# Kernel tuning notes

Hardware: AMD Instinct MI355X
Metric: run time of the kernel (lower is better)

The kernel has to match this reference:

```python
import jax, jax.numpy as jnp
import numpy as np

BATCH, SEQ, H, P, HID, CHUNK = 2, 2048, 32, 64, 2048, 256
NORM_EPS = 1e-5


def setup_inputs() -> dict:
    key = jax.random.key(0)
    ks = jax.random.split(key, 10)
    f = lambda k, sh, sc=1.0: jax.random.normal(k, sh, jnp.float32) * sc
    return {
        "hidden_states_ab": f(ks[0], (BATCH, SEQ, HID), 0.02),
        "hidden_states_g": f(ks[1], (BATCH, SEQ, HID), 0.02),
        "q_states": f(ks[2], (BATCH, SEQ, H, P)),
        "k_states": f(ks[3], (BATCH, SEQ, H, P)),
        "v_states": f(ks[4], (BATCH, SEQ, H, P)),
        "dt_w": f(ks[5], (HID, H), 0.02),
        "dt_b": jnp.zeros((H,), jnp.float32),
        "g_w": f(ks[6], (HID, H), 0.02),
        "g_b": jnp.zeros((H,), jnp.float32),
        "A_log": jnp.log(jnp.arange(1, H + 1, dtype=jnp.float32)),
        "dt_bias": jnp.ones((H,), jnp.float32),
        "norm_weight": jnp.ones((H * P,), jnp.float32),
        "o_w": f(ks[7], (H, P, P), 0.02),
        "o_b": jnp.zeros((H, P), jnp.float32),
    }


def _l2norm(x, eps=1e-12):
    # torch F.normalize(p=2, dim=-1): x / max(||x||, eps)
    n = jnp.sqrt(jnp.sum(x * x, axis=-1, keepdims=True))
    return x / jnp.maximum(n, eps)


def _ssd(x, dt, A, Bm, Cm, chunk):
    # x: (b,s,h,p)  dt: (b,s,h) post-softplus  A: (h,)  Bm/Cm: (b,s,h,n)
    b, s, h, p = x.shape
    n = Bm.shape[-1]
    c = s // chunk
    rs = lambda t: t.reshape(b, c, chunk, *t.shape[2:])
    x, dt, Bm, Cm = rs(x), rs(dt), rs(Bm), rs(Cm)
    a = dt * A                         # (b,c,L,h) log-decay increments
    cum = jnp.cumsum(a, axis=2)        # (b,c,L,h)
    cumT = jnp.swapaxes(cum, 2, 3)     # (b,c,h,L)
    # intra-chunk (quadratic, causal) part
    diff = cumT[..., :, None] - cumT[..., None, :]          # (b,c,h,L,L)
    mask = jnp.tril(jnp.ones((chunk, chunk), bool))
    decay = jnp.exp(jnp.where(mask, diff, -jnp.inf))
    CB = jnp.einsum('bclhn,bcshn->bchls', Cm, Bm)
    scores = CB * decay * jnp.swapaxes(dt, 2, 3)[:, :, :, None, :]
    y = jnp.einsum('bchls,bcshp->bclhp', scores, x)
    # per-chunk states
    decay_last = jnp.exp(cumT[..., -1:] - cumT)             # (b,c,h,L)
    w = jnp.swapaxes(decay_last, 2, 3) * dt                 # (b,c,L,h)
    states = jnp.einsum('bclh,bclhn,bclhp->bchpn', w, Bm, x)
    # inter-chunk recurrence over c chunks
    chunk_decay = jnp.exp(cumT[..., -1])                    # (b,c,h)
    def step(Hs, inp):
        cd, st = inp
        return cd[..., None, None] * Hs + st, Hs
    H_last, H_prev = jax.lax.scan(
        step, jnp.zeros((b, h, p, n), x.dtype),
        (jnp.moveaxis(chunk_decay, 1, 0), jnp.moveaxis(states, 1, 0)))
    H_prev = jnp.moveaxis(H_prev, 0, 1)                     # (b,c,h,p,n)
    y = y + jnp.einsum('bclhn,bclh,bchpn->bclhp', Cm, jnp.exp(cum), H_prev)
    return y.reshape(b, s, h, p), H_last


def reference(hidden_states_ab, hidden_states_g, q_states, k_states, v_states,
              dt_w, dt_b, g_w, g_b, A_log, dt_bias, norm_weight, o_w, o_b):
    b, s, h, p = v_states.shape
    Cm = _l2norm(q_states)
    Bm = _l2norm(k_states)
    # dt_proj bias + mamba dt_bias, then softplus (dt_softplus=True)
    dt = jax.nn.softplus(hidden_states_ab @ dt_w + dt_b + dt_bias)   # (b,s,h)
    A = -jnp.exp(A_log)
    y, ssm_state = _ssd(v_states, dt, A, Bm, Cm, CHUNK)
    # gate: g_proj then repeat_interleave(head_dim) on last dim
    gate = jnp.repeat(hidden_states_g @ g_w + g_b, p, axis=-1)       # (b,s,h*p)
    # RMSNormGated, norm_before_gate=False: normalize(x * silu(z)) * weight
    y = y.reshape(b, s, h * p) * jax.nn.silu(gate)
    y = y * jax.lax.rsqrt(jnp.mean(y * y, axis=-1, keepdims=True) + NORM_EPS)
    y = y * norm_weight
    # GroupLinear o_proj: per-head (p -> p) linear
    out = jnp.einsum('bshp,hpq->bshq', y.reshape(b, s, h, p), o_w) + o_b
    return out.reshape(b, s, h * p)
```

## Files before the change

kernel.cpp:

```cpp
#include <hip/hip_runtime.h>
#include <math.h>

#define BATCH 2
#define SEQ   2048
#define NH    32
#define HID   2048
#define CHUNK 256
#define NCH   8
#define NBCH  (BATCH*NCH*NH)
#define PST   72
#define BK    256
#define APST  264
#define KSPLIT 4
#define KSEG  (HID / KSPLIT)

typedef __attribute__((ext_vector_type(4))) float f32x4;
typedef __attribute__((ext_vector_type(8))) short bf16x8;
typedef unsigned int uint;
typedef unsigned short ushort;

__device__ __forceinline__ float softplusf(float x) {
    return x > 20.f ? x : log1pf(expf(x));
}

__device__ __forceinline__ short f2bf(float f) {
    union { float f; uint u; } v; v.f = f;
    uint r = v.u + 0x7FFF + ((v.u >> 16) & 1);
    return (short)(r >> 16);
}
__device__ __forceinline__ float bf2f(ushort s) {
    union { uint u; float f; } v; v.u = ((uint)s) << 16; return v.f;
}
__device__ __forceinline__ uint packbf2(float lo, float hi) {
    return (uint)(ushort)f2bf(lo) | ((uint)(ushort)f2bf(hi) << 16);
}

struct BF8 { union { bf16x8 v; short s[8]; }; };

__device__ __forceinline__ bf16x8 load_cvt8(const float* p, float scale) {
    float4 a = *(const float4*)p;
    float4 b = *(const float4*)(p + 4);
    BF8 r;
    r.s[0]=f2bf(a.x*scale); r.s[1]=f2bf(a.y*scale); r.s[2]=f2bf(a.z*scale); r.s[3]=f2bf(a.w*scale);
    r.s[4]=f2bf(b.x*scale); r.s[5]=f2bf(b.y*scale); r.s[6]=f2bf(b.z*scale); r.s[7]=f2bf(b.w*scale);
    return r.v;
}

__device__ __forceinline__ bf16x8 cvt8(float4 a, float4 b, float s) {
    BF8 r;
    r.s[0]=f2bf(a.x*s); r.s[1]=f2bf(a.y*s); r.s[2]=f2bf(a.z*s); r.s[3]=f2bf(a.w*s);
    r.s[4]=f2bf(b.x*s); r.s[5]=f2bf(b.y*s); r.s[6]=f2bf(b.z*s); r.s[7]=f2bf(b.w*s);
    return r.v;
}

#define MFMA(a,b,c) __builtin_amdgcn_mfma_f32_16x16x32_bf16((a),(b),(c),0,0,0)

__global__ __launch_bounds__(256) void k_proj(
    const float* __restrict__ hs_ab, const float* __restrict__ hs_g,
    const float* __restrict__ dt_w, const float* __restrict__ g_w,
    const float* __restrict__ o_w,  const float* __restrict__ norm_w,
    float* __restrict__ part, short* __restrict__ nwWT)
{
    __shared__ __align__(16) short As[32 * APST];
    __shared__ __align__(16) short Bs[32 * APST];
    int blk = blockIdx.x;
    int t = threadIdx.x;

    if (blk >= 2 * KSPLIT * 128) {
        int h = blk - 2 * KSPLIT * 128;
        float* tile = (float*)As;
        {
            int p = t >> 2, q0 = (t & 3) * 16;
            const float* wp = o_w + (size_t)h * 4096 + p * 64 + q0;
            #pragma unroll
            for (int i = 0; i < 4; ++i)
                *(float4*)(tile + p * 64 + q0 + i * 4) = *(const float4*)(wp + i * 4);
        }
        __syncthreads();
        int q = t >> 2, p0 = (t & 3) * 16;
        uint us[8];
        #pragma unroll
        for (int j = 0; j < 8; ++j) {
            float lo = tile[(p0 + 2*j    ) * 64 + q] * norm_w[h * 64 + p0 + 2*j];
            float hi = tile[(p0 + 2*j + 1) * 64 + q] * norm_w[h * 64 + p0 + 2*j + 1];
            us[j] = packbf2(lo, hi);
        }
        uint* dst = (uint*)(nwWT + (size_t)h * 4096 + q * 64 + p0);
        *(uint4*)dst       = make_uint4(us[0], us[1], us[2], us[3]);
        *(uint4*)(dst + 4) = make_uint4(us[4], us[5], us[6], us[7]);
        return;
    }

    int ksp = blk >> 8;
    int rem = blk & 255;
    int which = rem >> 7;
    int rt = rem & 127;
    int r0 = rt * 32;
    const float* Am = which ? hs_g : hs_ab;
    const float* W  = which ? g_w  : dt_w;
    int w = t >> 6, lane = t & 63, quad = lane >> 4, l16 = lane & 15;
    int mh = w & 1, nh = w >> 1;

    f32x4 acc = (f32x4){0.f, 0.f, 0.f, 0.f};

    for (int kc = ksp * KSEG; kc < ksp * KSEG + KSEG; kc += BK) {
        __syncthreads();
        {
            int row = t >> 3, k0 = (t & 7) * 32;
            const float* src = Am + (size_t)(r0 + row) * HID + kc + k0;
            uint* dst = (uint*)(As + row * APST + k0);
            #pragma unroll
            for (int i = 0; i < 4; ++i) {
                float4 a = *(const float4*)(src + i * 8);
                float4 b = *(const float4*)(src + i * 8 + 4);
                dst[i*4+0] = packbf2(a.x, a.y); dst[i*4+1] = packbf2(a.z, a.w);
                dst[i*4+2] = packbf2(b.x, b.y); dst[i*4+3] = packbf2(b.z, b.w);
            }
        }
        if (t < 128) {
            int k2 = t * 2;
            const float* w0 = W + (size_t)(kc + k2) * NH;
            const float* w1 = w0 + NH;
            #pragma unroll
            for (int n = 0; n < 32; n += 4) {
                float4 a = *(const float4*)(w0 + n);
                float4 b = *(const float4*)(w1 + n);
                *((uint*)(Bs + (n+0) * APST + k2)) = packbf2(a.x, b.x);
                *((uint*)(Bs + (n+1) * APST + k2)) = packbf2(a.y, b.y);
                *((uint*)(Bs + (n+2) * APST + k2)) = packbf2(a.z, b.z);
                *((uint*)(Bs + (n+3) * APST + k2)) = packbf2(a.w, b.w);
            }
        }
        __syncthreads();
        #pragma unroll
        for (int ks = 0; ks < BK / 32; ++ks) {
            bf16x8 af = *(const bf16x8*)(As + (mh*16 + l16) * APST + ks*32 + quad*8);
            bf16x8 bf = *(const bf16x8*)(Bs + (nh*16 + l16) * APST + ks*32 + quad*8);
            acc = MFMA(af, bf, acc);
        }
    }

    int n = nh * 16 + l16;
    int Rb = r0 + mh * 16 + quad * 4;
    float* pd = part + ((size_t)(which * KSPLIT + ksp) * 4096 + Rb) * 32 + n;
    #pragma unroll
    for (int r = 0; r < 4; ++r)
        pd[r * 32] = acc[r];
}

__global__ __launch_bounds__(256) void k_cumsum(
    const float* __restrict__ part, const float* __restrict__ dt_b,
    const float* __restrict__ dt_bias, const float* __restrict__ A_log,
    float* __restrict__ cumc, float* __restrict__ wvc,
    float* __restrict__ dtc, float* __restrict__ cd)
{
    __shared__ float wsum[4];
    int bch = blockIdx.x;
    int h = bch & 31, c = (bch >> 5) & 7, b = bch >> 8;
    int t = threadIdx.x;
    int w = t >> 6, lane = t & 63;
    int rid = (b * SEQ + c * CHUNK + t) * 32 + h;
    float s = part[rid] + part[131072 + rid] + part[262144 + rid] + part[393216 + rid];
    float dt_l = softplusf(s + dt_b[h] + dt_bias[h]);
    float A = -expf(A_log[h]);
    float v = dt_l * A;
    #pragma unroll
    for (int off = 1; off < 64; off <<= 1) {
        float u = __shfl_up(v, off);
        if (lane >= off) v += u;
    }
    if (lane == 63) wsum[w] = v;
    __syncthreads();
    float pre = 0.f;
    #pragma unroll
    for (int i = 0; i < 3; ++i)
        if (i < w) pre += wsum[i];
    float cum = v + pre;
    float tot = wsum[0] + wsum[1] + wsum[2] + wsum[3];
    size_t o = (size_t)bch * CHUNK + t;
    cumc[o] = cum;
    wvc[o] = expf(tot - cum) * dt_l;
    dtc[o] = dt_l;
    if (t == 255) cd[bch] = expf(tot);
}

__global__ __launch_bounds__(256) void k_states(
    const float* __restrict__ kst, const float* __restrict__ vst,
    const float* __restrict__ wvc, float* __restrict__ sp)
{
    __shared__ __align__(16) float kS[64 * 64];
    __shared__ __align__(16) float xS[64 * 64];
    int blk = blockIdx.x;
    int half = blk & 1, bch = blk >> 1;
    int h = bch & 31, c = (bch >> 5) & 7, b = bch >> 8;
    int t = threadIdx.x;
    size_t rowbase = (size_t)b * SEQ + c * CHUNK + half * 128;
    int pg = (t & 15) * 4, ng = (t >> 4) * 4;
    float acc[4][4];
    #pragma unroll
    for (int i = 0; i < 4; ++i)
        #pragma unroll
        for (int j = 0; j < 4; ++j) acc[i][j] = 0.f;

    for (int tt = 0; tt < 2; ++tt) {
        int r0 = t >> 4;
        int c4 = (t & 15) * 4;
        #pragma unroll
        for (int i = 0; i < 4; ++i) {
            int row = r0 + i * 16;
            size_t grow = (rowbase + tt * 64 + row) * NH + h;
            float wv = wvc[(size_t)bch * CHUNK + half * 128 + tt * 64 + row];
            float4 kv = *(const float4*)(kst + grow * 64 + c4);
            float4 xv = *(const float4*)(vst + grow * 64 + c4);
            float ssq = kv.x*kv.x + kv.y*kv.y + kv.z*kv.z + kv.w*kv.w;
            ssq += __shfl_xor(ssq, 1); ssq += __shfl_xor(ssq, 2);
            ssq += __shfl_xor(ssq, 4); ssq += __shfl_xor(ssq, 8);
            float ib = 1.f / fmaxf(sqrtf(ssq), 1e-12f);
            *(float4*)(kS + row * 64 + c4) =
                make_float4(kv.x * ib, kv.y * ib, kv.z * ib, kv.w * ib);
            *(float4*)(xS + row * 64 + c4) =
                make_float4(xv.x * wv, xv.y * wv, xv.z * wv, xv.w * wv);
        }
        __syncthreads();
        for (int ll = 0; ll < 64; ++ll) {
            float4 x4 = *(const float4*)(xS + ll * 64 + pg);
            float4 k4 = *(const float4*)(kS + ll * 64 + ng);
            acc[0][0] += x4.x * k4.x; acc[0][1] += x4.x * k4.y;
            acc[0][2] += x4.x * k4.z; acc[0][3] += x4.x * k4.w;
            acc[1][0] += x4.y * k4.x; acc[1][1] += x4.y * k4.y;
            acc[1][2] += x4.y * k4.z; acc[1][3] += x4.y * k4.w;
            acc[2][0] += x4.z * k4.x; acc[2][1] += x4.z * k4.y;
            acc[2][2] += x4.z * k4.z; acc[2][3] += x4.z * k4.w;
            acc[3][0] += x4.w * k4.x; acc[3][1] += x4.w * k4.y;
            acc[3][2] += x4.w * k4.z; acc[3][3] += x4.w * k4.w;
        }
        __syncthreads();
    }
    size_t obase = (size_t)blk * 4096;
    #pragma unroll
    for (int i = 0; i < 4; ++i)
        *(float4*)(sp + obase + (pg + i) * 64 + ng) =
            make_float4(acc[i][0], acc[i][1], acc[i][2], acc[i][3]);
}

__global__ __launch_bounds__(256) void k_scan(
    const float* __restrict__ sp, const float* __restrict__ cd,
    float* __restrict__ Hp)
{
    size_t id = (size_t)blockIdx.x * 256 + threadIdx.x;
    size_t bh = id >> 12, pn = id & 4095;
    size_t b = bh >> 5, h = bh & 31;
    float carry = 0.f;
    for (int c = 0; c < NCH; ++c) {
        size_t bch = (b * NCH + c) * NH + h;
        float st = sp[(bch * 2) * 4096 + pn] + sp[(bch * 2 + 1) * 4096 + pn];
        Hp[bch * 4096 + pn] = carry;
        carry = cd[bch] * carry + st;
    }
}

__global__ __launch_bounds__(256, 2) void k_intra(
    const float* __restrict__ qst, const float* __restrict__ kst,
    const float* __restrict__ vst,
    const float* __restrict__ cumc, const float* __restrict__ dtc,
    const float* __restrict__ Hp,
    short* __restrict__ ygb)
{
    __shared__ __align__(16) short B_s[64 * PST];
    __shared__ __align__(16) short XT_s[64 * PST];
    __shared__ __align__(16) short P_s[4 * 32 * PST];
    __shared__ float sCum[256];
    __shared__ float sDt[256];

    int blk = blockIdx.x;
    int grp = (blk < NBCH) ? 0 : 1;
    int bch = blk & (NBCH - 1);
    int h = bch & 31, c = (bch >> 5) & 7, b = bch >> 8;
    int t = threadIdx.x;
    int w = t >> 6, lane = t & 63;
    int quad = lane >> 4, l16 = lane & 15;
    int strip = grp ? (1 + (w & 1) + 4 * (w >> 1))
                    : (3 * (w & 1) + 4 * (w >> 1));
    size_t rowbase = (size_t)b * SEQ + c * CHUNK;

    sCum[t] = cumc[(size_t)bch * CHUNK + t];
    sDt[t]  = dtc[(size_t)bch * CHUNK + t];

    int ssA = t >> 2, q4A = (t & 3) * 16;
    int ss2 = t & 31, p0 = (t >> 5) * 8;

    bf16x8 cf[2][2];
    #pragma unroll
    for (int lt = 0; lt < 2; ++lt) {
        int l = strip * 32 + lt * 16 + l16;
        size_t grow = (rowbase + l) * NH + h;
        const float* qp = qst + grow * 64 + quad * 8;
        float4 a  = *(const float4*)qp;
        float4 bq = *(const float4*)(qp + 4);
        float4 c2 = *(const float4*)(qp + 32);
        float4 d  = *(const float4*)(qp + 36);
        float ssq = a.x*a.x + a.y*a.y + a.z*a.z + a.w*a.w
                  + bq.x*bq.x + bq.y*bq.y + bq.z*bq.z + bq.w*bq.w
                  + c2.x*c2.x + c2.y*c2.y + c2.z*c2.z + c2.w*c2.w
                  + d.x*d.x + d.y*d.y + d.z*d.z + d.w*d.w;
        ssq += __shfl_xor(ssq, 16);
        ssq += __shfl_xor(ssq, 32);
        float ic = 1.f / fmaxf(sqrtf(ssq), 1e-12f);
        cf[lt][0] = cvt8(a, bq, ic);
        cf[lt][1] = cvt8(c2, d, ic);
    }

    f32x4 acc[2][4];
    #pragma unroll
    for (int lt = 0; lt < 2; ++lt)
        #pragma unroll
        for (int pt = 0; pt < 4; ++pt)
            acc[lt][pt] = (f32x4){0.f, 0.f, 0.f, 0.f};

    {
        bf16x8 hf[4][2];
        #pragma unroll
        for (int pt = 0; pt < 4; ++pt) {
            const float* hp = Hp + (size_t)bch * 4096 + (pt * 16 + l16) * 64 + quad * 8;
            hf[pt][0] = load_cvt8(hp, 1.f);
            hf[pt][1] = load_cvt8(hp + 32, 1.f);
        }
        #pragma unroll
        for (int lt = 0; lt < 2; ++lt)
            #pragma unroll
            for (int pt = 0; pt < 4; ++pt) {
                acc[lt][pt] = MFMA(cf[lt][0], hf[pt][0], acc[lt][pt]);
                acc[lt][pt] = MFMA(cf[lt][1], hf[pt][1], acc[lt][pt]);
            }
    }
    __syncthreads();
    #pragma unroll
    for (int lt = 0; lt < 2; ++lt) {
        float e[4];
        #pragma unroll
        for (int r = 0; r < 4; ++r)
            e[r] = __expf(sCum[strip * 32 + lt * 16 + quad * 4 + r]);
        #pragma unroll
        for (int pt = 0; pt < 4; ++pt)
            #pragma unroll
            for (int r = 0; r < 4; ++r)
                acc[lt][pt][r] *= e[r];
    }

    short* Pw = P_s + w * 32 * PST;

    for (int st = 0; st < 4; ++st) {
        {
            size_t gK = (rowbase + st * 64 + ssA) * NH + h;
            const float4* kp = (const float4*)(kst + gK * 64 + q4A);
            float4 kv0 = kp[0], kv1 = kp[1], kv2 = kp[2], kv3 = kp[3];
            float ssq = kv0.x*kv0.x + kv0.y*kv0.y + kv0.z*kv0.z + kv0.w*kv0.w
                      + kv1.x*kv1.x + kv1.y*kv1.y + kv1.z*kv1.z + kv1.w*kv1.w
                      + kv2.x*kv2.x + kv2.y*kv2.y + kv2.z*kv2.z + kv2.w*kv2.w
                      + kv3.x*kv3.x + kv3.y*kv3.y + kv3.z*kv3.z + kv3.w*kv3.w;
            ssq += __shfl_xor(ssq, 1);
            ssq += __shfl_xor(ssq, 2);
            float ib = 1.f / fmaxf(sqrtf(ssq), 1e-12f);
            uint u[8];
            u[0] = packbf2(kv0.x * ib, kv0.y * ib); u[1] = packbf2(kv0.z * ib, kv0.w * ib);
            u[2] = packbf2(kv1.x * ib, kv1.y * ib); u[3] = packbf2(kv1.z * ib, kv1.w * ib);
            u[4] = packbf2(kv2.x * ib, kv2.y * ib); u[5] = packbf2(kv2.z * ib, kv2.w * ib);
            u[6] = packbf2(kv3.x * ib, kv3.y * ib); u[7] = packbf2(kv3.z * ib, kv3.w * ib);
            uint* dst = (uint*)(B_s + ssA * PST + q4A);
            *(uint4*)dst = make_uint4(u[0], u[1], u[2], u[3]);
            *(uint4*)(dst + 4) = make_uint4(u[4], u[5], u[6], u[7]);
        }
        {
            size_t g0 = (rowbase + st * 64 + 2 * ss2) * NH + h;
            const float* vp0 = vst + g0 * 64 + p0;
            const float* vp1 = vst + (g0 + NH) * 64 + p0;
            float4 xa0 = *(const float4*)vp0, xa1 = *(const float4*)(vp0 + 4);
            float4 xb0 = *(const float4*)vp1, xb1 = *(const float4*)(vp1 + 4);
            float dt0 = sDt[st * 64 + 2 * ss2];
            float dt1 = sDt[st * 64 + 2 * ss2 + 1];
            float x0[8] = {xa0.x, xa0.y, xa0.z, xa0.w, xa1.x, xa1.y, xa1.z, xa1.w};
            float x1[8] = {xb0.x, xb0.y, xb0.z, xb0.w, xb1.x, xb1.y, xb1.z, xb1.w};
            uint* xt = (uint*)XT_s;
            #pragma unroll
            for (int i = 0; i < 8; ++i)
                xt[(p0 + i) * (PST / 2) + ss2] = packbf2(x0[i] * dt0, x1[i] * dt1);
        }
        __syncthreads();

        if (strip * 32 + 31 >= st * 64) {
            bf16x8 xf[4][2];
            #pragma unroll
            for (int pt = 0; pt < 4; ++pt) {
                #pragma unroll
                for (int ks = 0; ks < 2; ++ks)
                    xf[pt][ks] = *(const bf16x8*)(XT_s + (pt * 16 + l16) * PST + ks * 32 + quad * 8);
            }

            #pragma unroll
            for (int lt = 0; lt < 2; ++lt) {
                int Lt = strip * 32 + lt * 16;
                float cl = sCum[Lt + l16];
                int lrow = lt * 16 + l16;
                #pragma unroll
                for (int mt = 0; mt < 4; ++mt) {
                    int S0 = st * 64 + mt * 16;
                    uint* pdst = (uint*)(Pw + lrow * PST + mt * 16 + quad * 4);
                    if (S0 > Lt + 15) {
                        *(uint2*)pdst = make_uint2(0u, 0u);
                        continue;
                    }
                    f32x4 sa = (f32x4){0.f, 0.f, 0.f, 0.f};
                    bf16x8 af0 = *(const bf16x8*)(B_s + (mt * 16 + l16) * PST + quad * 8);
                    bf16x8 af1 = *(const bf16x8*)(B_s + (mt * 16 + l16) * PST + 32 + quad * 8);
                    sa = MFMA(af0, cf[lt][0], sa);
                    sa = MFMA(af1, cf[lt][1], sa);
                    float vals[4];
                    #pragma unroll
                    for (int r = 0; r < 4; ++r) {
                        int s = S0 + quad * 4 + r;
                        float v = sa[r] * __expf(cl - sCum[s]);
                        vals[r] = (Lt + l16 >= s) ? v : 0.f;
                    }
                    *(uint2*)pdst = make_uint2(packbf2(vals[0], vals[1]),
                                               packbf2(vals[2], vals[3]));
                }
            }
            #pragma unroll
            for (int lt = 0; lt < 2; ++lt) {
                int Lmax = strip * 32 + lt * 16 + 15;
                #pragma unroll
                for (int ks = 0; ks < 2; ++ks) {
                    if (st * 64 + ks * 32 > Lmax) continue;
                    bf16x8 af = *(const bf16x8*)(Pw + (lt * 16 + l16) * PST + ks * 32 + quad * 8);
                    #pragma unroll
                    for (int pt = 0; pt < 4; ++pt)
                        acc[lt][pt] = MFMA(af, xf[pt][ks], acc[lt][pt]);
                }
            }
        }
        __syncthreads();
    }

    #pragma unroll
    for (int lt = 0; lt < 2; ++lt)
        #pragma unroll
        for (int pt = 0; pt < 4; ++pt)
            #pragma unroll
            for (int r = 0; r < 4; ++r) {
                int l = strip * 32 + lt * 16 + quad * 4 + r;
                int p = pt * 16 + l16;
                ygb[((rowbase + l) * NH + h) * 64 + p] = f2bf(acc[lt][pt][r]);
            }
}

__global__ __launch_bounds__(256) void k_out(
    const short* __restrict__ ygb, const float* __restrict__ part,
    const float* __restrict__ g_b, const short* __restrict__ nwWT,
    const float* __restrict__ o_b, float* __restrict__ out)
{
    __shared__ __align__(16) short yS[16 * 1024];
    __shared__ float silS[16 * 32];
    __shared__ float scaleS[16];
    int blk = blockIdx.x;
    int half = blk & 1, rt = blk >> 1;
    int r0 = rt * 16;
    int t = threadIdx.x;
    int w = t >> 6, lane = t & 63, quad = lane >> 4, l16 = lane & 15;

    const float* gpart = part + 4 * 131072;
    #pragma unroll
    for (int ii = 0; ii < 2; ++ii) {
        int idx = t + ii * 256;
        int rr = idx >> 5, hh = idx & 31;
        int rid = (r0 + rr) * 32 + hh;
        float g = gpart[rid] + gpart[131072 + rid] + gpart[262144 + rid]
                + gpart[393216 + rid] + g_b[hh];
        silS[idx] = g / (1.f + expf(-g));
    }
    __syncthreads();

    int r = t >> 4, cl = t & 15;
    const char* yrow = (const char*)(ygb + (size_t)(r0 + r) * 2048);
    float ssq = 0.f;
    #pragma unroll
    for (int i = 0; i < 16; ++i) {
        int cb = i * 256 + cl * 16;
        uint4 u = *(const uint4*)(yrow + cb);
        float s = silS[r * 32 + (cb >> 7)];
        float v0 = bf2f((ushort)(u.x & 0xFFFF)) * s, v1 = bf2f((ushort)(u.x >> 16)) * s;
        float v2 = bf2f((ushort)(u.y & 0xFFFF)) * s, v3 = bf2f((ushort)(u.y >> 16)) * s;
        float v4 = bf2f((ushort)(u.z & 0xFFFF)) * s, v5 = bf2f((ushort)(u.z >> 16)) * s;
        float v6 = bf2f((ushort)(u.w & 0xFFFF)) * s, v7 = bf2f((ushort)(u.w >> 16)) * s;
        ssq += v0*v0 + v1*v1 + v2*v2 + v3*v3 + v4*v4 + v5*v5 + v6*v6 + v7*v7;
        if ((cb >> 11) == half) {
            int cbl = cb & 2047;
            *(uint4*)((char*)yS + r * 2048 + (cbl ^ ((r & 7) << 4))) = u;
        }
    }
    ssq += __shfl_xor(ssq, 1); ssq += __shfl_xor(ssq, 2);
    ssq += __shfl_xor(ssq, 4); ssq += __shfl_xor(ssq, 8);
    if (cl == 0) scaleS[r] = rsqrtf(ssq / 2048.f + 1e-5f);
    __syncthreads();

    #pragma unroll
    for (int hh = 0; hh < 4; ++hh) {
        int h = half * 16 + w * 4 + hh;
        int hl = h & 15;
        const short* wb = nwWT + (size_t)h * 4096;
        bf16x8 bfr[4][2];
        #pragma unroll
        for (int nt = 0; nt < 4; ++nt)
            #pragma unroll
            for (int ks = 0; ks < 2; ++ks)
                bfr[nt][ks] = *(const bf16x8*)(wb + (nt * 16 + l16) * 64 + ks * 32 + quad * 8);
        bf16x8 af[2];
        #pragma unroll
        for (int ks = 0; ks < 2; ++ks) {
            int cbl = hl * 128 + ks * 64 + quad * 16;
            af[ks] = *(const bf16x8*)((const char*)yS + l16 * 2048 + (cbl ^ ((l16 & 7) << 4)));
        }
        f32x4 acc[4];
        #pragma unroll
        for (int nt = 0; nt < 4; ++nt) acc[nt] = (f32x4){0.f, 0.f, 0.f, 0.f};
        #pragma unroll
        for (int ks = 0; ks < 2; ++ks)
            #pragma unroll
            for (int nt = 0; nt < 4; ++nt)
                acc[nt] = MFMA(af[ks], bfr[nt][ks], acc[nt]);
        #pragma unroll
        for (int nt = 0; nt < 4; ++nt) {
            float bv = o_b[h * 64 + nt * 16 + l16];
            #pragma unroll
            for (int rr = 0; rr < 4; ++rr) {
                int row = quad * 4 + rr;
                float o = acc[nt][rr] * silS[row * 32 + h] * scaleS[row] + bv;
                out[(size_t)(r0 + row) * 2048 + h * 64 + nt * 16 + l16] = o;
            }
        }
    }
}

extern "C" void kernel_launch(void* const* d_in, const int* in_sizes, int n_in,
                              void* d_out, int out_size, void* d_ws, size_t ws_size,
                              hipStream_t stream) {
    const float* hs_ab   = (const float*)d_in[0];
    const float* hs_g    = (const float*)d_in[1];
    const float* qst     = (const float*)d_in[2];
    const float* kst     = (const float*)d_in[3];
    const float* vst     = (const float*)d_in[4];
    const float* dt_w    = (const float*)d_in[5];
    const float* dt_b    = (const float*)d_in[6];
    const float* g_w     = (const float*)d_in[7];
    const float* g_b     = (const float*)d_in[8];
    const float* A_log   = (const float*)d_in[9];
    const float* dt_bias = (const float*)d_in[10];
    const float* norm_w  = (const float*)d_in[11];
    const float* o_w     = (const float*)d_in[12];
    const float* o_b     = (const float*)d_in[13];
    float* out = (float*)d_out;

    float* ws = (float*)d_ws;
    size_t off = 0;
    float* part   = ws + off; off += (size_t)2 * KSPLIT * 4096 * 32;
    float* cumc   = ws + off; off += (size_t)NBCH * CHUNK;
    float* wvc    = ws + off; off += (size_t)NBCH * CHUNK;
    float* dtc    = ws + off; off += (size_t)NBCH * CHUNK;
    float* cd_ws  = ws + off; off += (size_t)NBCH;
    float* sp     = ws + off; off += (size_t)NBCH * 2 * 4096;
    float* Hp     = ws + off; off += (size_t)NBCH * 4096;
    short* nwWT   = (short*)(ws + off); off += (size_t)NH * 64 * 64 / 2;

    short* ygb = (short*)sp;

    k_proj<<<2 * KSPLIT * (BATCH * SEQ / 32) + NH, 256, 0, stream>>>(
        hs_ab, hs_g, dt_w, g_w, o_w, norm_w, part, nwWT);
    k_cumsum<<<NBCH, 256, 0, stream>>>(part, dt_b, dt_bias, A_log,
                                       cumc, wvc, dtc, cd_ws);
    k_states<<<NBCH * 2, 256, 0, stream>>>(kst, vst, wvc, sp);
    k_scan<<<BATCH * NH * 4096 / 256, 256, 0, stream>>>(sp, cd_ws, Hp);
    k_intra<<<NBCH * 2, 256, 0, stream>>>(qst, kst, vst, cumc, dtc, Hp, ygb);
    k_out<<<2 * (BATCH * SEQ / 16), 256, 0, stream>>>(ygb, part, g_b, nwWT, o_b, out);
}
```

Baseline: 276.1 us.

## Merge k_intra's two half-chunk blocks into one 512-thread block

k_intra previously launched two 256-thread blocks per (batch,chunk,head), each handling four of the eight 32-row strips. Both blocks loaded and normalized the same K and X tiles into shared memory. Now a single 512-thread block covers all eight strips, so each K/V tile is staged once and the per-thread staging work is halved. The cost is half as many blocks, a larger shared P buffer, and the triangular causal work now sitting inside one block, which may unbalance the waves.

```diff
diff --git a/kernel.cpp b/kernel.cpp
--- a/kernel.cpp
+++ b/kernel.cpp
@@ -259,7 +259,7 @@
     }
 }
 
-__global__ __launch_bounds__(256, 2) void k_intra(
+__global__ __launch_bounds__(512, 2) void k_intra(
     const float* __restrict__ qst, const float* __restrict__ kst,
     const float* __restrict__ vst,
     const float* __restrict__ cumc, const float* __restrict__ dtc,
@@ -268,26 +268,25 @@
 {
     __shared__ __align__(16) short B_s[64 * PST];
     __shared__ __align__(16) short XT_s[64 * PST];
-    __shared__ __align__(16) short P_s[4 * 32 * PST];
+    __shared__ __align__(16) short P_s[8 * 32 * PST];
     __shared__ float sCum[256];
     __shared__ float sDt[256];
 
-    int blk = blockIdx.x;
-    int grp = (blk < NBCH) ? 0 : 1;
-    int bch = blk & (NBCH - 1);
+    int bch = blockIdx.x;
     int h = bch & 31, c = (bch >> 5) & 7, b = bch >> 8;
     int t = threadIdx.x;
     int w = t >> 6, lane = t & 63;
     int quad = lane >> 4, l16 = lane & 15;
-    int strip = grp ? (1 + (w & 1) + 4 * (w >> 1))
-                    : (3 * (w & 1) + 4 * (w >> 1));
+    int strip = w;
     size_t rowbase = (size_t)b * SEQ + c * CHUNK;
 
-    sCum[t] = cumc[(size_t)bch * CHUNK + t];
-    sDt[t]  = dtc[(size_t)bch * CHUNK + t];
-
-    int ssA = t >> 2, q4A = (t & 3) * 16;
-    int ss2 = t & 31, p0 = (t >> 5) * 8;
+    if (t < 256) {
+        sCum[t] = cumc[(size_t)bch * CHUNK + t];
+        sDt[t]  = dtc[(size_t)bch * CHUNK + t];
+    }
+
+    int rowK = t >> 3, c8 = (t & 7) * 8;
+    int ss2 = t & 31, pg4 = (t >> 5) * 4;
 
     bf16x8 cf[2][2];
     #pragma unroll
@@ -351,39 +350,32 @@
 
     for (int st = 0; st < 4; ++st) {
         {
-            size_t gK = (rowbase + st * 64 + ssA) * NH + h;
-            const float4* kp = (const float4*)(kst + gK * 64 + q4A);
-            float4 kv0 = kp[0], kv1 = kp[1], kv2 = kp[2], kv3 = kp[3];
+            size_t gK = (rowbase + st * 64 + rowK) * NH + h;
+            const float4* kp = (const float4*)(kst + gK * 64 + c8);
+            float4 kv0 = kp[0], kv1 = kp[1];
             float ssq = kv0.x*kv0.x + kv0.y*kv0.y + kv0.z*kv0.z + kv0.w*kv0.w
-                      + kv1.x*kv1.x + kv1.y*kv1.y + kv1.z*kv1.z + kv1.w*kv1.w
-                      + kv2.x*kv2.x + kv2.y*kv2.y + kv2.z*kv2.z + kv2.w*kv2.w
-                      + kv3.x*kv3.x + kv3.y*kv3.y + kv3.z*kv3.z + kv3.w*kv3.w;
+                      + kv1.x*kv1.x + kv1.y*kv1.y + kv1.z*kv1.z + kv1.w*kv1.w;
             ssq += __shfl_xor(ssq, 1);
             ssq += __shfl_xor(ssq, 2);
+            ssq += __shfl_xor(ssq, 4);
             float ib = 1.f / fmaxf(sqrtf(ssq), 1e-12f);
-            uint u[8];
-            u[0] = packbf2(kv0.x * ib, kv0.y * ib); u[1] = packbf2(kv0.z * ib, kv0.w * ib);
-            u[2] = packbf2(kv1.x * ib, kv1.y * ib); u[3] = packbf2(kv1.z * ib, kv1.w * ib);
-            u[4] = packbf2(kv2.x * ib, kv2.y * ib); u[5] = packbf2(kv2.z * ib, kv2.w * ib);
-            u[6] = packbf2(kv3.x * ib, kv3.y * ib); u[7] = packbf2(kv3.z * ib, kv3.w * ib);
-            uint* dst = (uint*)(B_s + ssA * PST + q4A);
-            *(uint4*)dst = make_uint4(u[0], u[1], u[2], u[3]);
-            *(uint4*)(dst + 4) = make_uint4(u[4], u[5], u[6], u[7]);
+            uint u0 = packbf2(kv0.x * ib, kv0.y * ib);
+            uint u1 = packbf2(kv0.z * ib, kv0.w * ib);
+            uint u2 = packbf2(kv1.x * ib, kv1.y * ib);
+            uint u3 = packbf2(kv1.z * ib, kv1.w * ib);
+            *(uint4*)((uint*)(B_s + rowK * PST + c8)) = make_uint4(u0, u1, u2, u3);
         }
         {
             size_t g0 = (rowbase + st * 64 + 2 * ss2) * NH + h;
-            const float* vp0 = vst + g0 * 64 + p0;
-            const float* vp1 = vst + (g0 + NH) * 64 + p0;
-            float4 xa0 = *(const float4*)vp0, xa1 = *(const float4*)(vp0 + 4);
-            float4 xb0 = *(const float4*)vp1, xb1 = *(const float4*)(vp1 + 4);
+            float4 xa = *(const float4*)(vst + g0 * 64 + pg4);
+            float4 xb = *(const float4*)(vst + (g0 + NH) * 64 + pg4);
             float dt0 = sDt[st * 64 + 2 * ss2];
             float dt1 = sDt[st * 64 + 2 * ss2 + 1];
-            float x0[8] = {xa0.x, xa0.y, xa0.z, xa0.w, xa1.x, xa1.y, xa1.z, xa1.w};
-            float x1[8] = {xb0.x, xb0.y, xb0.z, xb0.w, xb1.x, xb1.y, xb1.z, xb1.w};
             uint* xt = (uint*)XT_s;
-            #pragma unroll
-            for (int i = 0; i < 8; ++i)
-                xt[(p0 + i) * (PST / 2) + ss2] = packbf2(x0[i] * dt0, x1[i] * dt1);
+            xt[(pg4 + 0) * (PST / 2) + ss2] = packbf2(xa.x * dt0, xb.x * dt1);
+            xt[(pg4 + 1) * (PST / 2) + ss2] = packbf2(xa.y * dt0, xb.y * dt1);
+            xt[(pg4 + 2) * (PST / 2) + ss2] = packbf2(xa.z * dt0, xb.z * dt1);
+            xt[(pg4 + 3) * (PST / 2) + ss2] = packbf2(xa.w * dt0, xb.w * dt1);
         }
         __syncthreads();
 
@@ -578,6 +570,6 @@
                                        cumc, wvc, dtc, cd_ws);
     k_states<<<NBCH * 2, 256, 0, stream>>>(kst, vst, wvc, sp);
     k_scan<<<BATCH * NH * 4096 / 256, 256, 0, stream>>>(sp, cd_ws, Hp);
-    k_intra<<<NBCH * 2, 256, 0, stream>>>(qst, kst, vst, cumc, dtc, Hp, ygb);
+    k_intra<<<NBCH, 512, 0, stream>>>(qst, kst, vst, cumc, dtc, Hp, ygb);
     k_out<<<2 * (BATCH * SEQ / 16), 256, 0, stream>>>(ygb, part, g_b, nwWT, o_b, out);
 }
```

After: 279.7 us. Within noise of the previous version (+1.3%).
